# Kernel optimization log

Hardware: AMD Instinct MI355X
Metric: run time of the kernel (lower is better)

The kernel has to match this reference:

```python
import jax, jax.numpy as jnp
import numpy as np

NEG_SLOPE = 0.2  # PyG GATConv LeakyReLU slope
HEADS = 4

def _gat_conv(x, edge_index, W, a_src, a_dst, b):
    """Single-relation GATConv (PyG semantics, concat=True).
    x: [N, Fin]; edge_index: [2, E]; W: [Fin, H*D]; a_src/a_dst: [H, D]; b: [H*D].
    """
    N = x.shape[0]
    H, D = a_src.shape
    h = (x @ W).reshape(N, H, D)                      # [N, H, D]
    src, dst = edge_index[0], edge_index[1]
    # per-node attention halves
    al_s = jnp.einsum('nhd,hd->nh', h, a_src)         # [N, H]
    al_d = jnp.einsum('nhd,hd->nh', h, a_dst)         # [N, H]
    alpha = jax.nn.leaky_relu(al_s[src] + al_d[dst], NEG_SLOPE)  # [E, H]
    # segment softmax over incoming edges per destination node
    amax = jax.ops.segment_max(alpha, dst, num_segments=N)       # [N, H]
    e = jnp.exp(alpha - amax[dst])
    denom = jax.ops.segment_sum(e, dst, num_segments=N)          # [N, H]
    w = e / (denom[dst] + 1e-16)                                  # [E, H]
    msg = h[src] * w[:, :, None]                                  # [E, H, D]
    out = jax.ops.segment_sum(msg, dst, num_segments=N)          # [N, H, D]
    return out.reshape(N, H * D) + b

def setup_inputs() -> dict:
    key = jax.random.key(0)
    ks = jax.random.split(key, 8)
    N, Fin, Fout, E, R = 50000, 256, 128, 800000, 3
    return {
        'x': jax.random.normal(ks[0], (N, Fin), dtype=jnp.float32),
        'edge_index_0': jax.random.randint(ks[1], (2, E), 0, N, dtype=jnp.int32),
        'edge_index_1': jax.random.randint(ks[2], (2, E), 0, N, dtype=jnp.int32),
        'edge_index_2': jax.random.randint(ks[3], (2, E), 0, N, dtype=jnp.int32),
        'W': jax.random.normal(ks[4], (R, Fin, Fout), dtype=jnp.float32) * 0.05,
        'att_src': jax.random.normal(ks[5], (R, HEADS, Fout // HEADS), dtype=jnp.float32) * 0.1,
        'att_dst': jax.random.normal(ks[6], (R, HEADS, Fout // HEADS), dtype=jnp.float32) * 0.1,
        'bias': jax.random.normal(ks[7], (R, Fout), dtype=jnp.float32) * 0.01,
    }

def reference(x, edge_index_0, edge_index_1, edge_index_2, W, att_src, att_dst, bias):
    edges = (edge_index_0, edge_index_1, edge_index_2)
    out = None
    for r in range(W.shape[0]):  # small fixed relation loop
        h_rel = _gat_conv(x, edges[r], W[r], att_src[r], att_dst[r], bias[r])
        out = h_rel if out is None else out + h_rel
    return out
```

## Files before the change

### kernel.cpp

```cpp
#include <hip/hip_runtime.h>
#include <hip/hip_bf16.h>

#define NEG_SLOPE 0.2f
#define NBMAX 320
#define KB    512
#define CAP   10240
#define CHUNK 4096

typedef short bf16x8 __attribute__((ext_vector_type(8)));
typedef float f32x4  __attribute__((ext_vector_type(4)));
typedef float f32x16 __attribute__((ext_vector_type(16)));

__device__ inline ushort f2bf(float f) {
  __hip_bfloat16 b = __float2bfloat16(f);
  return *(ushort*)&b;
}

__global__ __launch_bounds__(256)
void prep_kernel(const float* __restrict__ W,
                 const float* __restrict__ a_src,
                 const float* __restrict__ a_dst,
                 ushort* __restrict__ WbigT,
                 int* __restrict__ bcnt) {
  const int b = blockIdx.x;
  const int t = threadIdx.x;
  if (b == 448) {
    for (int k = t; k < NBMAX; k += 256) bcnt[k] = 0;
    return;
  }
  int i = b * 256 + t;
  int c = i >> 8, k = i & 255;
  float v = 0.f;
  if (c < 384) {
    int r = c >> 7, j = c & 127;
    v = W[((size_t)r * 256 + k) * 128 + j];
  } else if (c < 408) {
    int c6 = c - 384, r = c6 >> 3, hh = c6 & 7, hd = hh & 3;
    const float* a = (hh < 4 ? a_src : a_dst) + (r * 4 + hd) * 32;
    const float* wp = W + ((size_t)r * 256 + k) * 128 + hd * 32;
#pragma unroll
    for (int d = 0; d < 32; ++d) v += wp[d] * a[d];
  }
  WbigT[i] = f2bf(v);
}

__global__ __launch_bounds__(256, 2)
void gemm_mfma_kernel(const float* __restrict__ x, const ushort* __restrict__ WT,
                      ushort* __restrict__ hall, float* __restrict__ al, int M) {
  __shared__ __align__(16) ushort As[64][40];
  __shared__ __align__(16) ushort Bs[448][40];
  const int bm = blockIdx.x * 64;
  const int t = threadIdx.x;
  const int l = t & 63;
  const int w = t >> 6;
  const int wm = (w >> 1) * 32;
  const int wn = (w & 1) * 224;
  const int lr31 = l & 31;
  const int kg = (l >> 5) * 8;

  f32x16 acc[7];
#pragma unroll
  for (int j = 0; j < 7; ++j)
#pragma unroll
    for (int r = 0; r < 16; ++r) acc[j][r] = 0.f;

  for (int k0 = 0; k0 < 256; k0 += 32) {
    {
      int row = t >> 2, seg = t & 3;
      int grow = bm + row;
      float4 v0 = make_float4(0.f, 0.f, 0.f, 0.f), v1 = v0;
      if (grow < M) {
        const float* xp = x + (size_t)grow * 256 + k0 + seg * 8;
        v0 = *(const float4*)xp;
        v1 = *(const float4*)(xp + 4);
      }
      uint4 pk;
      pk.x = (unsigned)f2bf(v0.x) | ((unsigned)f2bf(v0.y) << 16);
      pk.y = (unsigned)f2bf(v0.z) | ((unsigned)f2bf(v0.w) << 16);
      pk.z = (unsigned)f2bf(v1.x) | ((unsigned)f2bf(v1.y) << 16);
      pk.w = (unsigned)f2bf(v1.z) | ((unsigned)f2bf(v1.w) << 16);
      *(uint4*)&As[row][seg * 8] = pk;
    }
#pragma unroll
    for (int p = 0; p < 7; ++p) {
      int idx = p * 256 + t;
      int nrow = idx >> 2, ch = idx & 3;
      *(uint4*)&Bs[nrow][ch * 8] =
          *(const uint4*)(WT + (size_t)nrow * 256 + k0 + ch * 8);
    }
    __syncthreads();

#pragma unroll
    for (int kk = 0; kk < 32; kk += 16) {
      bf16x8 af = *(bf16x8*)&As[wm + lr31][kk + kg];
#pragma unroll
      for (int j = 0; j < 7; ++j) {
        bf16x8 bf = *(bf16x8*)&Bs[wn + j * 32 + lr31][kk + kg];
        acc[j] = __builtin_amdgcn_mfma_f32_32x32x16_bf16(af, bf, acc[j], 0, 0, 0);
      }
    }
    __syncthreads();
  }

#pragma unroll
  for (int j = 0; j < 7; ++j) {
    int gcol = wn + j * 32 + lr31;
#pragma unroll
    for (int r = 0; r < 16; ++r) {
      int grow = bm + wm + (l >> 5) * 4 + (r & 3) + 8 * (r >> 2);
      if (grow >= M) continue;
      float c = acc[j][r];
      if (gcol < 384) {
        int rel = gcol >> 7, jj = gcol & 127;
        hall[((size_t)rel * M + grow) * 128 + jj] = f2bf(c);
      } else if (gcol < 408) {
        int c6 = gcol - 384, rr = c6 >> 3, hh = c6 & 7;
        al[(((size_t)(hh < 4 ? 0 : 3) + rr) * M + grow) * 4 + (hh & 3)] = c;
      }
    }
  }
}

__device__ inline void edge_decode(int i, int E0, int E1,
                                   const int* __restrict__ s0, const int* __restrict__ d0,
                                   const int* __restrict__ s1, const int* __restrict__ d1,
                                   const int* __restrict__ s2, const int* __restrict__ d2,
                                   int N, int& src, int& key) {
  if (i < E0)            { src = s0[i];            key = d0[i]; }
  else if (i < E0 + E1)  { src = s1[i - E0];       key = N + d1[i - E0]; }
  else                   { src = s2[i - E0 - E1];  key = 2 * N + d2[i - E0 - E1]; }
}

__global__ __launch_bounds__(512)
void bucket_stage(const int* __restrict__ s0, const int* __restrict__ d0,
                  const int* __restrict__ s1, const int* __restrict__ d1,
                  const int* __restrict__ s2, const int* __restrict__ d2,
                  int E0, int E1, int E2,
                  int* __restrict__ bcnt, unsigned* __restrict__ staging,
                  int N, int NB) {
  __shared__ ushort es_src[CHUNK];
  __shared__ int    es_key[CHUNK];
  __shared__ int lh[NBMAX], lb[NBMAX];
  const int t = threadIdx.x;
  for (int k = t; k < NB; k += 512) lh[k] = 0;
  __syncthreads();
  const int Etot = E0 + E1 + E2;
  const int lo = blockIdx.x * CHUNK;
  const int hi = min(lo + CHUNK, Etot);
  const int n = hi - lo;
  for (int i = t; i < n; i += 512) {
    int src, key;
    edge_decode(lo + i, E0, E1, s0, d0, s1, d1, s2, d2, N, src, key);
    es_src[i] = (ushort)src;
    es_key[i] = key;
    atomicAdd(&lh[key >> 9], 1);
  }
  __syncthreads();
  for (int k = t; k < NB; k += 512) {
    int v = lh[k];
    lb[k] = v ? (k * CAP + atomicAdd(&bcnt[k], v)) : 0;
    lh[k] = 0;
  }
  __syncthreads();
  for (int i = t; i < n; i += 512) {
    int key = es_key[i];
    int b = key >> 9;
    int pos = lb[b] + atomicAdd(&lh[b], 1);
    if (pos < (b + 1) * CAP)
      staging[pos] = ((unsigned)(key & 511) << 16) | (unsigned)es_src[i];
  }
}

__global__ __launch_bounds__(512)
void bucket_sort(const unsigned* __restrict__ staging, const int* __restrict__ bcnt,
                 int* __restrict__ offs, int* __restrict__ ends,
                 ushort* __restrict__ srt, int n3) {
  __shared__ int cnt[KB];
  __shared__ int cur[KB];
  __shared__ int wsum[8];
  const int b = blockIdx.x;
  const int base = b * KB;
  const int lo = b * CAP;
  const int t = threadIdx.x;
  const int lane = t & 63, wid = t >> 6;
  const int m = min(bcnt[b], CAP);
  cnt[t] = 0;
  __syncthreads();
  for (int i = t; i < m; i += 512)
    atomicAdd(&cnt[staging[lo + i] >> 16], 1);
  __syncthreads();
  int v = cnt[t];
  int sv = v;
#pragma unroll
  for (int d = 1; d < 64; d <<= 1) {
    int u = __shfl_up(sv, d);
    if (lane >= d) sv += u;
  }
  if (lane == 63) wsum[wid] = sv;
  __syncthreads();
  if (t < 8) {
    int ws = wsum[t];
#pragma unroll
    for (int d = 1; d < 8; d <<= 1) {
      int u = __shfl_up(ws, d);
      if (t >= d) ws += u;
    }
    wsum[t] = ws;
  }
  __syncthreads();
  int start = lo + (wid ? wsum[wid - 1] : 0) + sv - v;
  cur[t] = start;
  if (base + t < n3) {
    offs[base + t] = start;
    ends[base + t] = start + v;
  }
  __syncthreads();
  for (int i = t; i < m; i += 512) {
    unsigned p = staging[lo + i];
    int pos = atomicAdd(&cur[p >> 16], 1);
    srt[pos] = (ushort)(p & 0xffffu);
  }
}

__global__ __launch_bounds__(128)
void gat_fused_kernel(const ushort* __restrict__ srt, const int* __restrict__ offs,
                      const int* __restrict__ ends,
                      const ushort* __restrict__ hall,
                      const float* __restrict__ al,
                      const float* __restrict__ bias,
                      float* __restrict__ out, int N) {
  const int d = blockIdx.x;
  const int t = threadIdx.x;
  const int w = t >> 6;
  const int l = t & 63;
  const int eg = l >> 4;
  const int fl = l & 15;
  const int h = fl >> 2;

  __shared__ float slab[3][2][16][9];

#pragma unroll
  for (int rel = 0; rel < 3; ++rel) {
    const int key = rel * N + d;
    const int start = offs[key];
    const int dend = ends[key];
    const float* alS = al + (size_t)rel * N * 4;
    const ushort* hrel = hall + (size_t)rel * N * 128;
    const float ald = al[((size_t)(3 + rel) * N + d) * 4 + h];
    float r0 = 0.f, r1 = 0.f, r2 = 0.f, r3 = 0.f;
    float r4 = 0.f, r5 = 0.f, r6 = 0.f, r7 = 0.f;
    float dl = 0.f;
#pragma unroll 2
    for (int e = start + w * 4 + eg; e < dend; e += 8) {
      int s = srt[e];
      float a = alS[(size_t)s * 4 + h] + ald;
      a = fmaxf(a, NEG_SLOPE * a);
      float ex = __expf(a);
      dl += ex;
      uint4 u = *(const uint4*)(hrel + (size_t)s * 128 + fl * 8);
      r0 += __uint_as_float(u.x << 16) * ex;
      r1 += __uint_as_float(u.x & 0xffff0000u) * ex;
      r2 += __uint_as_float(u.y << 16) * ex;
      r3 += __uint_as_float(u.y & 0xffff0000u) * ex;
      r4 += __uint_as_float(u.z << 16) * ex;
      r5 += __uint_as_float(u.z & 0xffff0000u) * ex;
      r6 += __uint_as_float(u.w << 16) * ex;
      r7 += __uint_as_float(u.w & 0xffff0000u) * ex;
    }
    r0 += __shfl_xor(r0, 16); r0 += __shfl_xor(r0, 32);
    r1 += __shfl_xor(r1, 16); r1 += __shfl_xor(r1, 32);
    r2 += __shfl_xor(r2, 16); r2 += __shfl_xor(r2, 32);
    r3 += __shfl_xor(r3, 16); r3 += __shfl_xor(r3, 32);
    r4 += __shfl_xor(r4, 16); r4 += __shfl_xor(r4, 32);
    r5 += __shfl_xor(r5, 16); r5 += __shfl_xor(r5, 32);
    r6 += __shfl_xor(r6, 16); r6 += __shfl_xor(r6, 32);
    r7 += __shfl_xor(r7, 16); r7 += __shfl_xor(r7, 32);
    dl += __shfl_xor(dl, 16); dl += __shfl_xor(dl, 32);
    if (l < 16) {
      slab[rel][w][fl][0] = r0; slab[rel][w][fl][1] = r1;
      slab[rel][w][fl][2] = r2; slab[rel][w][fl][3] = r3;
      slab[rel][w][fl][4] = r4; slab[rel][w][fl][5] = r5;
      slab[rel][w][fl][6] = r6; slab[rel][w][fl][7] = r7;
      slab[rel][w][fl][8] = dl;
    }
  }
  __syncthreads();
  {
    int fl2 = t >> 3, k = t & 7;
    int f = fl2 * 8 + k;
    float o = bias[f] + bias[128 + f] + bias[256 + f];
#pragma unroll
    for (int rel = 0; rel < 3; ++rel) {
      float D = slab[rel][0][fl2][8] + slab[rel][1][fl2][8];
      float R = slab[rel][0][fl2][k] + slab[rel][1][fl2][k];
      o += R / (D + 1e-16f);
    }
    out[(size_t)d * 128 + f] = o;
  }
}

extern "C" void kernel_launch(void* const* d_in, const int* in_sizes, int n_in,
                              void* d_out, int out_size, void* d_ws, size_t ws_size,
                              hipStream_t stream) {
  const float* x     = (const float*)d_in[0];
  const int*   ei[3] = {(const int*)d_in[1], (const int*)d_in[2], (const int*)d_in[3]};
  const float* W     = (const float*)d_in[4];
  const float* a_src = (const float*)d_in[5];
  const float* a_dst = (const float*)d_in[6];
  const float* bias  = (const float*)d_in[7];

  const int Fin = 256;
  const int N = in_sizes[0] / Fin;
  const int E0 = in_sizes[1] / 2, E1 = in_sizes[2] / 2, E2 = in_sizes[3] / 2;
  const int Etot = E0 + E1 + E2;
  const int n3 = 3 * N;
  const int NB = (n3 + KB - 1) / KB;

  float* out = (float*)d_out;

  char* p = (char*)d_ws;
  ushort*   WbigT   = (ushort*)p;    p += (size_t)448 * 256 * 2;
  ushort*   hall    = (ushort*)p;    p += (size_t)N * 384 * 2;
  float*    al      = (float*)p;     p += (size_t)6 * N * 4 * 4;
  unsigned* staging = (unsigned*)p;  p += (size_t)NBMAX * CAP * 4;
  ushort*   srt     = (ushort*)p;    p += (size_t)NBMAX * CAP * 2;
  int*      offs    = (int*)p;       p += (size_t)n3 * 4;
  int*      ends    = (int*)p;       p += (size_t)n3 * 4;
  int*      bcnt    = (int*)p;       p += NBMAX * 4;

  prep_kernel<<<449, 256, 0, stream>>>(W, a_src, a_dst, WbigT, bcnt);

  gemm_mfma_kernel<<<(N + 63) / 64, 256, 0, stream>>>(x, WbigT, hall, al, N);

  bucket_stage<<<(Etot + CHUNK - 1) / CHUNK, 512, 0, stream>>>(
      ei[0], ei[0] + E0, ei[1], ei[1] + E1, ei[2], ei[2] + E2,
      E0, E1, E2, bcnt, staging, N, NB);

  bucket_sort<<<NB, 512, 0, stream>>>(staging, bcnt, offs, ends, srt, n3);

  gat_fused_kernel<<<N, 128, 0, stream>>>(srt, offs, ends, hall, al, bias, out, N);
}
```

Baseline: 212.9 us.

## Merge GEMM and edge bucket staging into one launch with block-role split

The separate MFMA projection GEMM and edge bucketing kernels become one launch, where the first GB blocks run the GEMM and the rest run bucket staging, sharing a union shared-memory buffer. The two independent stages can then run concurrently on the GPU and one launch gap is removed. In exchange, staging blocks drop from 512 to 256 threads and inherit the GEMM's larger shared-memory footprint and register pressure under launch_bounds(256,2), which may lower their occupancy.

```diff
diff --git a/kernel.cpp b/kernel.cpp
--- a/kernel.cpp
+++ b/kernel.cpp
@@ -44,83 +44,6 @@
   WbigT[i] = f2bf(v);
 }
 
-__global__ __launch_bounds__(256, 2)
-void gemm_mfma_kernel(const float* __restrict__ x, const ushort* __restrict__ WT,
-                      ushort* __restrict__ hall, float* __restrict__ al, int M) {
-  __shared__ __align__(16) ushort As[64][40];
-  __shared__ __align__(16) ushort Bs[448][40];
-  const int bm = blockIdx.x * 64;
-  const int t = threadIdx.x;
-  const int l = t & 63;
-  const int w = t >> 6;
-  const int wm = (w >> 1) * 32;
-  const int wn = (w & 1) * 224;
-  const int lr31 = l & 31;
-  const int kg = (l >> 5) * 8;
-
-  f32x16 acc[7];
-#pragma unroll
-  for (int j = 0; j < 7; ++j)
-#pragma unroll
-    for (int r = 0; r < 16; ++r) acc[j][r] = 0.f;
-
-  for (int k0 = 0; k0 < 256; k0 += 32) {
-    {
-      int row = t >> 2, seg = t & 3;
-      int grow = bm + row;
-      float4 v0 = make_float4(0.f, 0.f, 0.f, 0.f), v1 = v0;
-      if (grow < M) {
-        const float* xp = x + (size_t)grow * 256 + k0 + seg * 8;
-        v0 = *(const float4*)xp;
-        v1 = *(const float4*)(xp + 4);
-      }
-      uint4 pk;
-      pk.x = (unsigned)f2bf(v0.x) | ((unsigned)f2bf(v0.y) << 16);
-      pk.y = (unsigned)f2bf(v0.z) | ((unsigned)f2bf(v0.w) << 16);
-      pk.z = (unsigned)f2bf(v1.x) | ((unsigned)f2bf(v1.y) << 16);
-      pk.w = (unsigned)f2bf(v1.z) | ((unsigned)f2bf(v1.w) << 16);
-      *(uint4*)&As[row][seg * 8] = pk;
-    }
-#pragma unroll
-    for (int p = 0; p < 7; ++p) {
-      int idx = p * 256 + t;
-      int nrow = idx >> 2, ch = idx & 3;
-      *(uint4*)&Bs[nrow][ch * 8] =
-          *(const uint4*)(WT + (size_t)nrow * 256 + k0 + ch * 8);
-    }
-    __syncthreads();
-
-#pragma unroll
-    for (int kk = 0; kk < 32; kk += 16) {
-      bf16x8 af = *(bf16x8*)&As[wm + lr31][kk + kg];
-#pragma unroll
-      for (int j = 0; j < 7; ++j) {
-        bf16x8 bf = *(bf16x8*)&Bs[wn + j * 32 + lr31][kk + kg];
-        acc[j] = __builtin_amdgcn_mfma_f32_32x32x16_bf16(af, bf, acc[j], 0, 0, 0);
-      }
-    }
-    __syncthreads();
-  }
-
-#pragma unroll
-  for (int j = 0; j < 7; ++j) {
-    int gcol = wn + j * 32 + lr31;
-#pragma unroll
-    for (int r = 0; r < 16; ++r) {
-      int grow = bm + wm + (l >> 5) * 4 + (r & 3) + 8 * (r >> 2);
-      if (grow >= M) continue;
-      float c = acc[j][r];
-      if (gcol < 384) {
-        int rel = gcol >> 7, jj = gcol & 127;
-        hall[((size_t)rel * M + grow) * 128 + jj] = f2bf(c);
-      } else if (gcol < 408) {
-        int c6 = gcol - 384, rr = c6 >> 3, hh = c6 & 7;
-        al[(((size_t)(hh < 4 ? 0 : 3) + rr) * M + grow) * 4 + (hh & 3)] = c;
-      }
-    }
-  }
-}
-
 __device__ inline void edge_decode(int i, int E0, int E1,
                                    const int* __restrict__ s0, const int* __restrict__ d0,
                                    const int* __restrict__ s1, const int* __restrict__ d1,
@@ -131,43 +54,129 @@
   else                   { src = s2[i - E0 - E1];  key = 2 * N + d2[i - E0 - E1]; }
 }
 
-__global__ __launch_bounds__(512)
-void bucket_stage(const int* __restrict__ s0, const int* __restrict__ d0,
-                  const int* __restrict__ s1, const int* __restrict__ d1,
-                  const int* __restrict__ s2, const int* __restrict__ d2,
-                  int E0, int E1, int E2,
-                  int* __restrict__ bcnt, unsigned* __restrict__ staging,
-                  int N, int NB) {
-  __shared__ ushort es_src[CHUNK];
-  __shared__ int    es_key[CHUNK];
-  __shared__ int lh[NBMAX], lb[NBMAX];
+struct GemmSmem {
+  ushort As[64][40];
+  ushort Bs[448][40];
+};
+struct StageSmem {
+  ushort es_src[CHUNK];
+  int    es_key[CHUNK];
+  int    lh[NBMAX];
+  int    lb[NBMAX];
+};
+
+__global__ __launch_bounds__(256, 2)
+void gemm_stage_kernel(const float* __restrict__ x, const ushort* __restrict__ WT,
+                       ushort* __restrict__ hall, float* __restrict__ al, int M,
+                       const int* __restrict__ s0, const int* __restrict__ d0,
+                       const int* __restrict__ s1, const int* __restrict__ d1,
+                       const int* __restrict__ s2, const int* __restrict__ d2,
+                       int E0, int E1, int E2,
+                       int* __restrict__ bcnt, unsigned* __restrict__ staging,
+                       int N, int NB, int GB) {
+  __shared__ __align__(16) char smem_raw[sizeof(GemmSmem) > sizeof(StageSmem)
+                                             ? sizeof(GemmSmem) : sizeof(StageSmem)];
   const int t = threadIdx.x;
-  for (int k = t; k < NB; k += 512) lh[k] = 0;
-  __syncthreads();
-  const int Etot = E0 + E1 + E2;
-  const int lo = blockIdx.x * CHUNK;
-  const int hi = min(lo + CHUNK, Etot);
-  const int n = hi - lo;
-  for (int i = t; i < n; i += 512) {
-    int src, key;
-    edge_decode(lo + i, E0, E1, s0, d0, s1, d1, s2, d2, N, src, key);
-    es_src[i] = (ushort)src;
-    es_key[i] = key;
-    atomicAdd(&lh[key >> 9], 1);
-  }
-  __syncthreads();
-  for (int k = t; k < NB; k += 512) {
-    int v = lh[k];
-    lb[k] = v ? (k * CAP + atomicAdd(&bcnt[k], v)) : 0;
-    lh[k] = 0;
-  }
-  __syncthreads();
-  for (int i = t; i < n; i += 512) {
-    int key = es_key[i];
-    int b = key >> 9;
-    int pos = lb[b] + atomicAdd(&lh[b], 1);
-    if (pos < (b + 1) * CAP)
-      staging[pos] = ((unsigned)(key & 511) << 16) | (unsigned)es_src[i];
+
+  if (blockIdx.x < GB) {
+    GemmSmem& sm = *reinterpret_cast<GemmSmem*>(smem_raw);
+    const int bm = blockIdx.x * 64;
+    const int l = t & 63;
+    const int w = t >> 6;
+    const int wm = (w >> 1) * 32;
+    const int wn = (w & 1) * 224;
+    const int lr31 = l & 31;
+    const int kg = (l >> 5) * 8;
+
+    f32x16 acc[7];
+#pragma unroll
+    for (int j = 0; j < 7; ++j)
+#pragma unroll
+      for (int r = 0; r < 16; ++r) acc[j][r] = 0.f;
+
+    for (int k0 = 0; k0 < 256; k0 += 32) {
+      {
+        int row = t >> 2, seg = t & 3;
+        int grow = bm + row;
+        float4 v0 = make_float4(0.f, 0.f, 0.f, 0.f), v1 = v0;
+        if (grow < M) {
+          const float* xp = x + (size_t)grow * 256 + k0 + seg * 8;
+          v0 = *(const float4*)xp;
+          v1 = *(const float4*)(xp + 4);
+        }
+        uint4 pk;
+        pk.x = (unsigned)f2bf(v0.x) | ((unsigned)f2bf(v0.y) << 16);
+        pk.y = (unsigned)f2bf(v0.z) | ((unsigned)f2bf(v0.w) << 16);
+        pk.z = (unsigned)f2bf(v1.x) | ((unsigned)f2bf(v1.y) << 16);
+        pk.w = (unsigned)f2bf(v1.z) | ((unsigned)f2bf(v1.w) << 16);
+        *(uint4*)&sm.As[row][seg * 8] = pk;
+      }
+#pragma unroll
+      for (int p = 0; p < 7; ++p) {
+        int idx = p * 256 + t;
+        int nrow = idx >> 2, ch = idx & 3;
+        *(uint4*)&sm.Bs[nrow][ch * 8] =
+            *(const uint4*)(WT + (size_t)nrow * 256 + k0 + ch * 8);
+      }
+      __syncthreads();
+#pragma unroll
+      for (int kk = 0; kk < 32; kk += 16) {
+        bf16x8 af = *(bf16x8*)&sm.As[wm + lr31][kk + kg];
+#pragma unroll
+        for (int j = 0; j < 7; ++j) {
+          bf16x8 bf = *(bf16x8*)&sm.Bs[wn + j * 32 + lr31][kk + kg];
+          acc[j] = __builtin_amdgcn_mfma_f32_32x32x16_bf16(af, bf, acc[j], 0, 0, 0);
+        }
+      }
+      __syncthreads();
+    }
+
+#pragma unroll
+    for (int j = 0; j < 7; ++j) {
+      int gcol = wn + j * 32 + lr31;
+#pragma unroll
+      for (int r = 0; r < 16; ++r) {
+        int grow = bm + wm + (l >> 5) * 4 + (r & 3) + 8 * (r >> 2);
+        if (grow >= M) continue;
+        float c = acc[j][r];
+        if (gcol < 384) {
+          int rel = gcol >> 7, jj = gcol & 127;
+          hall[((size_t)rel * M + grow) * 128 + jj] = f2bf(c);
+        } else if (gcol < 408) {
+          int c6 = gcol - 384, rr = c6 >> 3, hh = c6 & 7;
+          al[(((size_t)(hh < 4 ? 0 : 3) + rr) * M + grow) * 4 + (hh & 3)] = c;
+        }
+      }
+    }
+  } else {
+    StageSmem& sm = *reinterpret_cast<StageSmem*>(smem_raw);
+    for (int k = t; k < NB; k += 256) sm.lh[k] = 0;
+    __syncthreads();
+    const int Etot = E0 + E1 + E2;
+    const int lo = (blockIdx.x - GB) * CHUNK;
+    const int hi = min(lo + CHUNK, Etot);
+    const int n = hi - lo;
+    for (int i = t; i < n; i += 256) {
+      int src, key;
+      edge_decode(lo + i, E0, E1, s0, d0, s1, d1, s2, d2, N, src, key);
+      sm.es_src[i] = (ushort)src;
+      sm.es_key[i] = key;
+      atomicAdd(&sm.lh[key >> 9], 1);
+    }
+    __syncthreads();
+    for (int k = t; k < NB; k += 256) {
+      int v = sm.lh[k];
+      sm.lb[k] = v ? (k * CAP + atomicAdd(&bcnt[k], v)) : 0;
+      sm.lh[k] = 0;
+    }
+    __syncthreads();
+    for (int i = t; i < n; i += 256) {
+      int key = sm.es_key[i];
+      int b = key >> 9;
+      int pos = sm.lb[b] + atomicAdd(&sm.lh[b], 1);
+      if (pos < (b + 1) * CAP)
+        staging[pos] = ((unsigned)(key & 511) << 16) | (unsigned)sm.es_src[i];
+    }
   }
 }
 
@@ -315,6 +324,8 @@
   const int Etot = E0 + E1 + E2;
   const int n3 = 3 * N;
   const int NB = (n3 + KB - 1) / KB;
+  const int GB = (N + 63) / 64;
+  const int SB = (Etot + CHUNK - 1) / CHUNK;
 
   float* out = (float*)d_out;
 
@@ -330,11 +341,10 @@
 
   prep_kernel<<<449, 256, 0, stream>>>(W, a_src, a_dst, WbigT, bcnt);
 
-  gemm_mfma_kernel<<<(N + 63) / 64, 256, 0, stream>>>(x, WbigT, hall, al, N);
-
-  bucket_stage<<<(Etot + CHUNK - 1) / CHUNK, 512, 0, stream>>>(
+  gemm_stage_kernel<<<GB + SB, 256, 0, stream>>>(
+      x, WbigT, hall, al, N,
       ei[0], ei[0] + E0, ei[1], ei[1] + E1, ei[2], ei[2] + E2,
-      E0, E1, E2, bcnt, staging, N, NB);
+      E0, E1, E2, bcnt, staging, N, NB, GB);
 
   bucket_sort<<<NB, 512, 0, stream>>>(staging, bcnt, offs, ends, srt, n3);
 
```

Result: faster. 199.6 us (-6.3%).
